# Kernel optimization log

Hardware: AMD Instinct MI355X
Metric: run time of the kernel (lower is better)

## Reference

```python
import jax, jax.numpy as jnp
from jax import lax
import numpy as np

B, S, H, DIN, BIN, NH, NL = 32, 256, 256, 16, 2, 8, 3
DH = H // NH


def setup_inputs() -> dict:
    key = jax.random.key(0)
    it = iter(jax.random.split(key, 40))
    def nrm(shape, s=0.05):
        return jax.random.normal(next(it), shape, jnp.float32) * s
    return {
        "parts": jax.random.normal(next(it), (B, S, DIN), jnp.float32),
        "bin_info": jax.random.normal(next(it), (B, BIN), jnp.float32),
        "target": jax.random.randint(next(it), (B, S), 0, S, dtype=jnp.int32),
        "pe_W1": nrm((H // 2, DIN)), "pe_b1": jnp.zeros((H // 2,), jnp.float32),
        "pe_W2": nrm((H // 2, H // 2)), "pe_b2": jnp.zeros((H // 2,), jnp.float32),
        "be_W1": nrm((H // 4, BIN)), "be_b1": jnp.zeros((H // 4,), jnp.float32),
        "be_W2": nrm((H // 4, H // 4)), "be_b2": jnp.zeros((H // 4,), jnp.float32),
        "pos_emb": nrm((S, H // 4)),
        "tr_Wqkv": nrm((NL, 3 * H, H)), "tr_bqkv": jnp.zeros((NL, 3 * H), jnp.float32),
        "tr_Wo": nrm((NL, H, H)), "tr_bo": jnp.zeros((NL, H), jnp.float32),
        "tr_ln1_g": jnp.ones((NL, H), jnp.float32), "tr_ln1_b": jnp.zeros((NL, H), jnp.float32),
        "tr_ff_W1": nrm((NL, 2 * H, H)), "tr_ff_b1": jnp.zeros((NL, 2 * H), jnp.float32),
        "tr_ff_W2": nrm((NL, H, 2 * H)), "tr_ff_b2": jnp.zeros((NL, H), jnp.float32),
        "tr_ln2_g": jnp.ones((NL, H), jnp.float32), "tr_ln2_b": jnp.zeros((NL, H), jnp.float32),
        "lstm_Wih": nrm((4 * H, H)), "lstm_Whh": nrm((4 * H, H)),
        "lstm_bih": jnp.zeros((4 * H,), jnp.float32), "lstm_bhh": jnp.zeros((4 * H,), jnp.float32),
        "ptr_W": nrm((H, H)), "ptr_b": jnp.zeros((H,), jnp.float32),
        "ptr_v": nrm((H,)),
    }


def _ln(x, g, b):
    m = x.mean(-1, keepdims=True)
    v = ((x - m) ** 2).mean(-1, keepdims=True)
    return (x - m) / jnp.sqrt(v + 1e-5) * g + b


def _forward(parts, bin_info, target, pe_W1, pe_b1, pe_W2, pe_b2,
             be_W1, be_b1, be_W2, be_b2, pos_emb,
             tr_Wqkv, tr_bqkv, tr_Wo, tr_bo, tr_ln1_g, tr_ln1_b,
             tr_ff_W1, tr_ff_b1, tr_ff_W2, tr_ff_b2, tr_ln2_g, tr_ln2_b,
             lstm_Wih, lstm_Whh, lstm_bih, lstm_bhh, ptr_W, ptr_b, ptr_v):
    # --- encode_inputs (dropout inactive in eval) ---
    p = jax.nn.relu(parts @ pe_W1.T + pe_b1) @ pe_W2.T + pe_b2            # [B,S,H/2]
    bb = jax.nn.relu(bin_info @ be_W1.T + be_b1) @ be_W2.T + be_b2        # [B,H/4]
    bb = jnp.broadcast_to(bb[:, None, :], (B, S, H // 4))
    pe = jnp.broadcast_to(pos_emb[None], (B, S, H // 4))
    x = jnp.concatenate([p, bb, pe], axis=-1)                             # [B,S,H]
    scale = 1.0 / np.sqrt(DH)
    for l in range(NL):  # post-norm TransformerEncoderLayer, relu FFN
        qkv = x @ tr_Wqkv[l].T + tr_bqkv[l]
        q, k, v = jnp.split(qkv, 3, axis=-1)
        q = q.reshape(B, S, NH, DH).transpose(0, 2, 1, 3)
        k = k.reshape(B, S, NH, DH).transpose(0, 2, 1, 3)
        v = v.reshape(B, S, NH, DH).transpose(0, 2, 1, 3)
        a = jax.nn.softmax(jnp.einsum('bhqd,bhkd->bhqk', q, k) * scale, axis=-1)
        o = jnp.einsum('bhqk,bhkd->bhqd', a, v).transpose(0, 2, 1, 3).reshape(B, S, H)
        x = _ln(x + o @ tr_Wo[l].T + tr_bo[l], tr_ln1_g[l], tr_ln1_b[l])
        ff = jax.nn.relu(x @ tr_ff_W1[l].T + tr_ff_b1[l]) @ tr_ff_W2[l].T + tr_ff_b2[l]
        x = _ln(x + ff, tr_ln2_g[l], tr_ln2_b[l])
    enc = x
    # Note: the original's inner MultiheadAttention calls never feed the
    # returned step_logits (part_logit is overwritten), so the faithful output is
    # logits[b,t,i] = v . tanh(ptr(h_t) + ptr(enc_i)), vectorized over i here.
    e_proj = enc @ ptr_W.T + ptr_b                                        # [B,S,H]
    bidx = jnp.arange(B)

    def step(carry, tgt_t):
        h, c, xin = carry
        g = xin @ lstm_Wih.T + lstm_bih + h @ lstm_Whh.T + lstm_bhh
        i, f, gg, o = jnp.split(g, 4, axis=-1)
        c = jax.nn.sigmoid(f) * c + jax.nn.sigmoid(i) * jnp.tanh(gg)
        h = jax.nn.sigmoid(o) * jnp.tanh(c)
        hp = h @ ptr_W.T + ptr_b                                          # [B,H]
        logits = jnp.tanh(hp[:, None, :] + e_proj) @ ptr_v                # [B,S]
        nxt = enc[bidx, tgt_t]                                            # teacher forcing
        return (h, c, nxt), logits

    z = jnp.zeros((B, H), jnp.float32)
    _, logits = lax.scan(step, (z, z, z), target.T)                       # [S,B,S]
    return logits.transpose(1, 0, 2)                                      # [B,S,S]


def reference(parts, bin_info, target, pe_W1, pe_b1, pe_W2, pe_b2,
              be_W1, be_b1, be_W2, be_b2, pos_emb,
              tr_Wqkv, tr_bqkv, tr_Wo, tr_bo, tr_ln1_g, tr_ln1_b,
              tr_ff_W1, tr_ff_b1, tr_ff_W2, tr_ff_b2, tr_ln2_g, tr_ln2_b,
              lstm_Wih, lstm_Whh, lstm_bih, lstm_bhh, ptr_W, ptr_b, ptr_v):
    return _forward(parts, bin_info, target, pe_W1, pe_b1, pe_W2, pe_b2,
                    be_W1, be_b1, be_W2, be_b2, pos_emb,
                    tr_Wqkv, tr_bqkv, tr_Wo, tr_bo, tr_ln1_g, tr_ln1_b,
                    tr_ff_W1, tr_ff_b1, tr_ff_W2, tr_ff_b2, tr_ln2_g, tr_ln2_b,
                    lstm_Wih, lstm_Whh, lstm_bih, lstm_bhh, ptr_W, ptr_b, ptr_v)
```

## Files before the change

kernel.cpp:

```cpp
#include <hip/hip_runtime.h>
#include <cstddef>

#define DEV __device__ __forceinline__

DEV float fexp2(float x) { return __builtin_amdgcn_exp2f(x); }
DEV float frcp(float x)  { return __builtin_amdgcn_rcpf(x); }
DEV float fsigm(float x) { return frcp(1.0f + fexp2(-1.44269504f * x)); }
DEV float ftanh_(float x){ return 1.0f - 2.0f * frcp(1.0f + fexp2(2.88539008f * x)); }

typedef _Float16 h2t __attribute__((ext_vector_type(2)));
typedef _Float16 v8h __attribute__((ext_vector_type(8)));
typedef float v4f __attribute__((ext_vector_type(4)));
union U32H2 { unsigned int u; h2t h; };
DEV h2t u2h(unsigned int u) { U32H2 x; x.u = u; return x.h; }

template <int BM, int BN, bool RELU, bool OUTF16>
__global__ __launch_bounds__(256) void hgemm_kernel(
    const _Float16* __restrict__ A, const _Float16* __restrict__ W,
    const float* __restrict__ bias1, const float* __restrict__ bias2,
    void* __restrict__ Cout, int M, int N, int K)
{
    constexpr int MT = BM / 32;
    constexpr int NT = BN / 32;
    constexpr int RA = BM / 64;
    constexpr int RB = BN / 64;
    __shared__ _Float16 As[BM * 32];
    __shared__ _Float16 Bs[BN * 32];

    const int tid = threadIdx.x;
    const int lane = tid & 63;
    const int lm = lane & 15, lq = lane >> 4;
    const int wrow = ((tid >> 6) & 1) * (BM / 2);
    const int wcol = (tid >> 7) * (BN / 2);
    const int m0 = blockIdx.x * BM, n0 = blockIdx.y * BN;
    const _Float16* Ab = A + (size_t)m0 * K;
    const _Float16* Wb = W + (size_t)n0 * K;

    v4f acc[MT][NT];
#pragma unroll
    for (int i = 0; i < MT; ++i)
#pragma unroll
        for (int j = 0; j < NT; ++j) acc[i][j] = (v4f){0.f, 0.f, 0.f, 0.f};

    const int rowS = tid >> 2, qS = tid & 3;

    uint4 ra[RA], rb[RB];
#pragma unroll
    for (int r = 0; r < RA; ++r)
        ra[r] = *(const uint4*)(Ab + (size_t)(rowS + 64 * r) * K + qS * 8);
#pragma unroll
    for (int r = 0; r < RB; ++r)
        rb[r] = *(const uint4*)(Wb + (size_t)(rowS + 64 * r) * K + qS * 8);

    for (int k0 = 0; k0 < K; k0 += 32) {
        __syncthreads();
#pragma unroll
        for (int r = 0; r < RA; ++r)
            *(uint4*)(As + (size_t)(tid + 256 * r) * 8) = ra[r];
#pragma unroll
        for (int r = 0; r < RB; ++r)
            *(uint4*)(Bs + (size_t)(tid + 256 * r) * 8) = rb[r];
        __syncthreads();
        int kn = k0 + 32;
        if (kn < K) {
#pragma unroll
            for (int r = 0; r < RA; ++r)
                ra[r] = *(const uint4*)(Ab + (size_t)(rowS + 64 * r) * K + kn + qS * 8);
#pragma unroll
            for (int r = 0; r < RB; ++r)
                rb[r] = *(const uint4*)(Wb + (size_t)(rowS + 64 * r) * K + kn + qS * 8);
        }
        v8h af[MT], bf[NT];
#pragma unroll
        for (int i = 0; i < MT; ++i)
            af[i] = *(const v8h*)(As + (size_t)(wrow + i * 16 + lm) * 32 + lq * 8);
#pragma unroll
        for (int j = 0; j < NT; ++j)
            bf[j] = *(const v8h*)(Bs + (size_t)(wcol + j * 16 + lm) * 32 + lq * 8);
#pragma unroll
        for (int i = 0; i < MT; ++i)
#pragma unroll
            for (int j = 0; j < NT; ++j)
                acc[i][j] = __builtin_amdgcn_mfma_f32_16x16x32_f16(
                    af[i], bf[j], acc[i][j], 0, 0, 0);
    }

#pragma unroll
    for (int j = 0; j < NT; ++j) {
        int col = n0 + wcol + j * 16 + lm;
        float bv = bias1[col];
        if (bias2) bv += bias2[col];
#pragma unroll
        for (int i = 0; i < MT; ++i) {
            int rbase = m0 + wrow + i * 16 + lq * 4;
#pragma unroll
            for (int rg = 0; rg < 4; ++rg) {
                float vv = acc[i][j][rg] + bv;
                if (RELU) vv = fmaxf(vv, 0.f);
                if (OUTF16)
                    ((_Float16*)Cout)[(size_t)(rbase + rg) * N + col] = (_Float16)vv;
                else
                    ((float*)Cout)[(size_t)(rbase + rg) * N + col] = vv;
            }
        }
    }
}

__global__ __launch_bounds__(256) void hgemm_ln_kernel(
    const _Float16* __restrict__ A, const _Float16* __restrict__ W,
    const float* __restrict__ bias, const float* __restrict__ gamma,
    const float* __restrict__ beta, float* __restrict__ X,
    _Float16* __restrict__ X16, int K)
{
    constexpr int BM = 64, BN = 256, MT = 2, NT = 8, RA = 1, RB = 4;
    __shared__ _Float16 As[BM * 32];
    __shared__ _Float16 Bs[BN * 32];
    __shared__ float redS[2][BM][2];

    const int tid = threadIdx.x;
    const int lane = tid & 63;
    const int lm = lane & 15, lq = lane >> 4;
    const int wrow = ((tid >> 6) & 1) * 32;
    const int wcol = (tid >> 7) * 128;
    const int half = tid >> 7;
    const int m0 = blockIdx.x * BM;
    const _Float16* Ab = A + (size_t)m0 * K;

    v4f acc[MT][NT];
#pragma unroll
    for (int i = 0; i < MT; ++i)
#pragma unroll
        for (int j = 0; j < NT; ++j) acc[i][j] = (v4f){0.f, 0.f, 0.f, 0.f};

    const int rowS = tid >> 2, qS = tid & 3;

    uint4 ra[RA], rb[RB];
#pragma unroll
    for (int r = 0; r < RA; ++r)
        ra[r] = *(const uint4*)(Ab + (size_t)(rowS + 64 * r) * K + qS * 8);
#pragma unroll
    for (int r = 0; r < RB; ++r)
        rb[r] = *(const uint4*)(W + (size_t)(rowS + 64 * r) * K + qS * 8);

    for (int k0 = 0; k0 < K; k0 += 32) {
        __syncthreads();
#pragma unroll
        for (int r = 0; r < RA; ++r)
            *(uint4*)(As + (size_t)(tid + 256 * r) * 8) = ra[r];
#pragma unroll
        for (int r = 0; r < RB; ++r)
            *(uint4*)(Bs + (size_t)(tid + 256 * r) * 8) = rb[r];
        __syncthreads();
        int kn = k0 + 32;
        if (kn < K) {
#pragma unroll
            for (int r = 0; r < RA; ++r)
                ra[r] = *(const uint4*)(Ab + (size_t)(rowS + 64 * r) * K + kn + qS * 8);
#pragma unroll
            for (int r = 0; r < RB; ++r)
                rb[r] = *(const uint4*)(W + (size_t)(rowS + 64 * r) * K + kn + qS * 8);
        }
        v8h af[MT], bf[NT];
#pragma unroll
        for (int i = 0; i < MT; ++i)
            af[i] = *(const v8h*)(As + (size_t)(wrow + i * 16 + lm) * 32 + lq * 8);
#pragma unroll
        for (int j = 0; j < NT; ++j)
            bf[j] = *(const v8h*)(Bs + (size_t)(wcol + j * 16 + lm) * 32 + lq * 8);
#pragma unroll
        for (int i = 0; i < MT; ++i)
#pragma unroll
            for (int j = 0; j < NT; ++j)
                acc[i][j] = __builtin_amdgcn_mfma_f32_16x16x32_f16(
                    af[i], bf[j], acc[i][j], 0, 0, 0);
    }

    float s[MT][4], s2[MT][4];
#pragma unroll
    for (int i = 0; i < MT; ++i)
#pragma unroll
        for (int rg = 0; rg < 4; ++rg) { s[i][rg] = 0.f; s2[i][rg] = 0.f; }
#pragma unroll
    for (int j = 0; j < NT; ++j) {
        int col = wcol + j * 16 + lm;
        float bv = bias[col];
#pragma unroll
        for (int i = 0; i < MT; ++i) {
            int rbase = m0 + wrow + i * 16 + lq * 4;
#pragma unroll
            for (int rg = 0; rg < 4; ++rg) {
                float y = acc[i][j][rg] + bv + X[(size_t)(rbase + rg) * 256 + col];
                acc[i][j][rg] = y;
                s[i][rg] += y;
                s2[i][rg] += y * y;
            }
        }
    }
#pragma unroll
    for (int i = 0; i < MT; ++i)
#pragma unroll
        for (int rg = 0; rg < 4; ++rg) {
            float a = s[i][rg], b2 = s2[i][rg];
#pragma unroll
            for (int m = 1; m < 16; m <<= 1) {
                a += __shfl_xor(a, m);
                b2 += __shfl_xor(b2, m);
            }
            if (lm == 0) {
                int rloc = wrow + i * 16 + lq * 4 + rg;
                redS[half][rloc][0] = a;
                redS[half][rloc][1] = b2;
            }
        }
    __syncthreads();
#pragma unroll
    for (int i = 0; i < MT; ++i) {
#pragma unroll
        for (int rg = 0; rg < 4; ++rg) {
            int rloc = wrow + i * 16 + lq * 4 + rg;
            float st = redS[0][rloc][0] + redS[1][rloc][0];
            float s2t = redS[0][rloc][1] + redS[1][rloc][1];
            float mean = st * (1.f / 256.f);
            float var = s2t * (1.f / 256.f) - mean * mean;
            float inv = rsqrtf(var + 1e-5f);
            size_t rowb = (size_t)(m0 + rloc) * 256;
#pragma unroll
            for (int j = 0; j < NT; ++j) {
                int col = wcol + j * 16 + lm;
                float o = (acc[i][j][rg] - mean) * inv * gamma[col] + beta[col];
                X[rowb + col] = o;
                X16[rowb + col] = (_Float16)o;
            }
        }
    }
}

__global__ __launch_bounds__(256) void cvt_fused_kernel(
    const float* __restrict__ s0, const float* __restrict__ s1,
    const float* __restrict__ s2, const float* __restrict__ s3,
    const float* __restrict__ s4, const float* __restrict__ s5,
    _Float16* __restrict__ dst,
    const float* __restrict__ Whh, unsigned int* __restrict__ WB,
    const float* __restrict__ bih, const float* __restrict__ bhh,
    float* __restrict__ PB)
{
    if (blockIdx.x < 7424) {
        int i = blockIdx.x * 256 + threadIdx.x;
        if (i >= 1900544) return;
        float val;
        if (i < 589824)       val = s0[i];
        else if (i < 786432)  val = s1[i - 589824];
        else if (i < 1179648) val = s2[i - 786432];
        else if (i < 1572864) val = s3[i - 1179648];
        else if (i < 1835008) {
            int idx = i - 1572864;
            int rp = idx >> 8, k = idx & 255;
            int j = rp >> 2, g = rp & 3;
            val = s4[(g * 256 + j) * 256 + k];
        }
        else                  val = s5[i - 1835008];
        dst[i] = (_Float16)val;
    } else {
        int idx = (blockIdx.x - 7424) * 256 + threadIdx.x;
        if (idx < 1024) {
            int j = idx >> 2, g = idx & 3;
            PB[idx] = bih[g * 256 + j] + bhh[g * 256 + j];
        }
        int l = idx & 3;
        int gt = idx >> 2;
        int tid = gt & 511;
        int q = gt >> 9;
        int i, c;
        if (q < 8)       { i = q >> 1; c = q & 1; }
        else if (q < 52) { int qq = q - 8; i = qq / 11; c = 2 + qq % 11; }
        else             { int qq = q - 52; c = 13 + (qq >> 2); i = qq & 3; }
        int r = ((tid & 255) << 2) + i;
        int k = ((tid >> 8) << 7) + (c << 3) + (l << 1);
        _Float16 lo = (_Float16)Whh[r * 256 + k];
        _Float16 hi = (_Float16)Whh[r * 256 + k + 1];
        U32H2 x; x.h = h2t{lo, hi};
        WB[idx] = x.u;
    }
}

__global__ __launch_bounds__(128) void part_enc_kernel(
    const float* __restrict__ parts, const float* __restrict__ W1,
    const float* __restrict__ b1, const float* __restrict__ W2,
    const float* __restrict__ b2, const float* __restrict__ bin_info,
    const float* __restrict__ be_W1, const float* __restrict__ be_b1,
    const float* __restrict__ be_W2, const float* __restrict__ be_b2,
    const float* __restrict__ pos_emb, float* __restrict__ X,
    _Float16* __restrict__ X16)
{
    __shared__ float W2s[128][129];
    __shared__ float h1[128];
    __shared__ float pin[16];
    __shared__ float h1b[64];
    __shared__ float bb_s[64];
    int tid = threadIdx.x;
    int b = blockIdx.x >> 3, s0 = (blockIdx.x & 7) * 32;
    for (int l = 0; l < 128; ++l) W2s[l][tid] = W2[l * 128 + tid];
    {
        float x0 = bin_info[b * 2], x1 = bin_info[b * 2 + 1];
        if (tid < 64)
            h1b[tid] = fmaxf(be_W1[tid * 2] * x0 + be_W1[tid * 2 + 1] * x1
                             + be_b1[tid], 0.f);
        __syncthreads();
        if (tid < 64) {
            float a = be_b2[tid];
#pragma unroll 4
            for (int e = 0; e < 64; ++e) a += be_W2[tid * 64 + e] * h1b[e];
            bb_s[tid] = a;
        }
        __syncthreads();
    }
    float w1r[16];
#pragma unroll
    for (int k = 0; k < 16; ++k) w1r[k] = W1[tid * 16 + k];
    float bias1v = b1[tid], bias2v = b2[tid];
    for (int si = 0; si < 32; ++si) {
        int s = s0 + si;
        size_t row = (size_t)b * 256 + s;
        if (tid < 16) pin[tid] = parts[row * 16 + tid];
        __syncthreads();
        float h = bias1v;
#pragma unroll
        for (int k = 0; k < 16; ++k) h += w1r[k] * pin[k];
        h1[tid] = fmaxf(h, 0.f);
        __syncthreads();
        float acc = bias2v;
#pragma unroll 4
        for (int e = 0; e < 128; ++e) acc += W2s[tid][e] * h1[e];
        X[row * 256 + tid] = acc;
        X16[row * 256 + tid] = (_Float16)acc;
        if (tid < 64) {
            float bbv = bb_s[tid];
            float pev = pos_emb[s * 64 + tid];
            X[row * 256 + 128 + tid] = bbv;
            X[row * 256 + 192 + tid] = pev;
            X16[row * 256 + 128 + tid] = (_Float16)bbv;
            X16[row * 256 + 192 + tid] = (_Float16)pev;
        }
        __syncthreads();
    }
}

__global__ __launch_bounds__(256) void attn_mfma_kernel(
    const _Float16* __restrict__ QKV, _Float16* __restrict__ O16)
{
    int bh = blockIdx.x;
    int b = bh >> 3, h = bh & 7;
    const int tid = threadIdx.x;
    const int w = tid >> 6;
    const int lane = tid & 63;
    const int lm = lane & 15, lq = lane >> 4;
    const float c_se = 0.17677669529663687f * 1.44269504f;

    __shared__ _Float16 Ks[4][256][8];
    __shared__ _Float16 Vt[32][264];
    __shared__ _Float16 Ps[4][16][264];

    const _Float16* qkvb = QKV + (size_t)(b * 256) * 768 + h * 32;
    {
        int s = tid;
        const _Float16* kr = qkvb + (size_t)s * 768 + 256;
#pragma unroll
        for (int c = 0; c < 4; ++c)
            *(uint4*)&Ks[c][s][0] = *(const uint4*)(kr + c * 8);
        const _Float16* vr = qkvb + (size_t)s * 768 + 512;
        _Float16 vtmp[32];
        *(uint4*)&vtmp[0]  = *(const uint4*)(vr);
        *(uint4*)&vtmp[8]  = *(const uint4*)(vr + 8);
        *(uint4*)&vtmp[16] = *(const uint4*)(vr + 16);
        *(uint4*)&vtmp[24] = *(const uint4*)(vr + 24);
#pragma unroll
        for (int d = 0; d < 32; ++d) Vt[d][s] = vtmp[d];
    }
    __syncthreads();

#pragma unroll 1
    for (int st = 0; st < 4; ++st) {
        int rt = w * 4 + st;
        v8h qf = *(const v8h*)(QKV + (size_t)(b * 256 + rt * 16 + lm) * 768
                               + h * 32 + lq * 8);
        v4f acc[16];
#pragma unroll
        for (int ct = 0; ct < 16; ++ct) {
            v8h kf = *(const v8h*)&Ks[lq][ct * 16 + lm][0];
            acc[ct] = __builtin_amdgcn_mfma_f32_16x16x32_f16(
                qf, kf, (v4f){0.f, 0.f, 0.f, 0.f}, 0, 0, 0);
        }
        float sminv[4];
#pragma unroll
        for (int r = 0; r < 4; ++r) {
            float m = acc[0][r];
#pragma unroll
            for (int ct = 1; ct < 16; ++ct) m = fmaxf(m, acc[ct][r]);
#pragma unroll
            for (int msk = 1; msk < 16; msk <<= 1)
                m = fmaxf(m, __shfl_xor(m, msk));
            float ssum = 0.f;
#pragma unroll
            for (int ct = 0; ct < 16; ++ct) {
                float e = fexp2((acc[ct][r] - m) * c_se);
                acc[ct][r] = e;
                ssum += e;
            }
#pragma unroll
            for (int msk = 1; msk < 16; msk <<= 1)
                ssum += __shfl_xor(ssum, msk);
            sminv[r] = frcp(ssum);
        }
#pragma unroll
        for (int ct = 0; ct < 16; ++ct)
#pragma unroll
            for (int r = 0; r < 4; ++r)
                Ps[w][lq * 4 + r][ct * 16 + lm] =
                    (_Float16)(acc[ct][r] * sminv[r]);
#pragma unroll
        for (int dt = 0; dt < 2; ++dt) {
            v4f o = (v4f){0.f, 0.f, 0.f, 0.f};
#pragma unroll
            for (int jc = 0; jc < 8; ++jc) {
                v8h pf = *(const v8h*)&Ps[w][lm][jc * 32 + lq * 8];
                v8h vf = *(const v8h*)&Vt[dt * 16 + lm][jc * 32 + lq * 8];
                o = __builtin_amdgcn_mfma_f32_16x16x32_f16(pf, vf, o, 0, 0, 0);
            }
#pragma unroll
            for (int r = 0; r < 4; ++r)
                O16[(size_t)(b * 256 + rt * 16 + lq * 4 + r) * 256
                    + h * 32 + dt * 16 + lm] = (_Float16)o[r];
        }
    }
}

__global__ __launch_bounds__(256) void gather_kernel(
    const float* __restrict__ X, const int* __restrict__ target,
    _Float16* __restrict__ Xg16)
{
    int row = blockIdx.x;
    int b = row >> 8, t = row & 255;
    int d = threadIdx.x;
    float val = 0.f;
    if (t > 0) {
        int src = target[b * 256 + t - 1];
        val = X[((size_t)b * 256 + src) * 256 + d];
    }
    Xg16[(size_t)row * 256 + d] = (_Float16)val;
}

__global__ __launch_bounds__(512) void lstm_kernel(
    const _Float16* __restrict__ g_in, const uint4* __restrict__ WB4,
    _Float16* __restrict__ HALL16)
{
    const int b = blockIdx.x;
    const int tid = threadIdx.x;
    const int kh = tid >> 8, j4 = tid & 255;

    __shared__ uint4 WL4[4096];
    __shared__ float gpart[2][1024];
    __shared__ uint4 h2v[32];
    unsigned int* h2_s = (unsigned int*)h2v;

#pragma unroll
    for (int g = 0; g < 8; ++g) WL4[g * 512 + tid] = WB4[g * 512 + tid];
    uint4 wr[44];
#pragma unroll
    for (int q = 0; q < 44; ++q) wr[q] = WB4[(8 + q) * 512 + tid];
    if (tid < 128) h2_s[tid] = 0u;

    const _Float16* ginb = g_in + (size_t)b * 256 * 1024;
    uint2 gi = make_uint2(0u, 0u);
    if (tid < 256) gi = *(const uint2*)(ginb + tid * 4);
    float c_state = 0.f;
    const uint4* SW4 = WB4 + 52 * 512;
    __syncthreads();

    for (int t = 0; t < 256; ++t) {
        uint4 sw[12];
#pragma unroll
        for (int q = 0; q < 4; ++q) sw[q] = SW4[q * 512 + tid];

        unsigned int hword = h2_s[(kh << 6) + (tid & 63)];

        float acc[4] = {0.f, 0.f, 0.f, 0.f};
#pragma unroll
        for (int c = 0; c < 16; ++c) {
            if (c == 2) {
#pragma unroll
                for (int q = 4; q < 8; ++q) sw[q] = SW4[q * 512 + tid];
            }
            if (c == 6) {
#pragma unroll
                for (int q = 8; q < 12; ++q) sw[q] = SW4[q * 512 + tid];
            }
            h2t hx = u2h((unsigned int)__builtin_amdgcn_readlane((int)hword, 4 * c + 0));
            h2t hy = u2h((unsigned int)__builtin_amdgcn_readlane((int)hword, 4 * c + 1));
            h2t hz = u2h((unsigned int)__builtin_amdgcn_readlane((int)hword, 4 * c + 2));
            h2t hw = u2h((unsigned int)__builtin_amdgcn_readlane((int)hword, 4 * c + 3));
#pragma unroll
            for (int i = 0; i < 4; ++i) {
                uint4 w = (c < 2)  ? WL4[((i << 1) + c) * 512 + tid]
                        : (c < 13) ? wr[i * 11 + (c - 2)]
                                   : sw[((c - 13) << 2) + i];
                acc[i] = __builtin_amdgcn_fdot2(u2h(w.x), hx, acc[i], false);
                acc[i] = __builtin_amdgcn_fdot2(u2h(w.y), hy, acc[i], false);
                acc[i] = __builtin_amdgcn_fdot2(u2h(w.z), hz, acc[i], false);
                acc[i] = __builtin_amdgcn_fdot2(u2h(w.w), hw, acc[i], false);
            }
        }
        *(float4*)&gpart[kh][j4 << 2] = make_float4(acc[0], acc[1], acc[2], acc[3]);
        __syncthreads();

        if (tid < 256) {
            int j = tid;
            h2t p0 = u2h(gi.x), p1 = u2h(gi.y);
            float ig = (float)p0.x + gpart[0][j]       + gpart[1][j];
            float fg = (float)p0.y + gpart[0][j + 256] + gpart[1][j + 256];
            float gg = (float)p1.x + gpart[0][j + 512] + gpart[1][j + 512];
            float og = (float)p1.y + gpart[0][j + 768] + gpart[1][j + 768];
            c_state = fsigm(fg) * c_state + fsigm(ig) * ftanh_(gg);
            float h = fsigm(og) * ftanh_(c_state);
            HALL16[((size_t)(b * 256 + t)) * 256 + j] = (_Float16)h;
            U32H2 hxp; hxp.h = h2t{(_Float16)h, (_Float16)0.f};
            unsigned int hu = hxp.u & 0xffffu;
            unsigned int other = (unsigned int)__shfl_xor((int)hu, 1);
            if ((j & 1) == 0) h2_s[j >> 1] = hu | (other << 16);
            int tn = (t < 255) ? (t + 1) : 255;
            gi = *(const uint2*)(ginb + (size_t)tn * 1024 + j * 4);
        }
        __syncthreads();
    }
}

__global__ __launch_bounds__(256) void pointer_kernel(
    const float* __restrict__ HP, const float* __restrict__ EP,
    const float* __restrict__ v, float* __restrict__ out)
{
    int b = blockIdx.z, tt = blockIdx.y, it = blockIdx.x;
    __shared__ float hp_s[16][260];
    __shared__ float ep_s[16][260];
    __shared__ float v_s[256];
    __shared__ float red[4];
    int tid = threadIdx.x;
    const float cs = 2.88539008f;
    const float* hpb = HP + ((size_t)b * 256 + tt * 16) * 256;
    const float* epb = EP + ((size_t)b * 256 + it * 16) * 256;
#pragma unroll
    for (int l = 0; l < 4; ++l) {
        int idx = tid + l * 256;
        int r = idx >> 6, c4 = idx & 63;
        float4 hv = *(const float4*)(hpb + r * 256 + c4 * 4);
        hv.x *= cs; hv.y *= cs; hv.z *= cs; hv.w *= cs;
        *(float4*)&hp_s[r][c4 * 4] = hv;
        float4 ev = *(const float4*)(epb + r * 256 + c4 * 4);
        ev.x *= cs; ev.y *= cs; ev.z *= cs; ev.w *= cs;
        *(float4*)&ep_s[r][c4 * 4] = ev;
    }
    float vv = v[tid];
    v_s[tid] = vv;
    float vp = vv;
#pragma unroll
    for (int m = 1; m < 64; m <<= 1) vp += __shfl_xor(vp, m);
    if ((tid & 63) == 0) red[tid >> 6] = vp;
    __syncthreads();
    float vsum = red[0] + red[1] + red[2] + red[3];
    int tl = tid >> 4, il = tid & 15;
    float acc = 0.f;
#pragma unroll 4
    for (int d = 0; d < 256; ++d) {
        float sval = hp_s[tl][d] + ep_s[il][d];
        float r = frcp(1.0f + fexp2(sval));
        acc = fmaf(v_s[d], r, acc);
    }
    out[((size_t)b * 256 + tt * 16 + tl) * 256 + it * 16 + il] =
        vsum - 2.0f * acc;
}

extern "C" void kernel_launch(void* const* d_in, const int* in_sizes, int n_in,
                              void* d_out, int out_size, void* d_ws, size_t ws_size,
                              hipStream_t stream)
{
    const float* parts    = (const float*)d_in[0];
    const float* bin_info = (const float*)d_in[1];
    const int*   target   = (const int*)d_in[2];
    const float* pe_W1 = (const float*)d_in[3];
    const float* pe_b1 = (const float*)d_in[4];
    const float* pe_W2 = (const float*)d_in[5];
    const float* pe_b2 = (const float*)d_in[6];
    const float* be_W1 = (const float*)d_in[7];
    const float* be_b1 = (const float*)d_in[8];
    const float* be_W2 = (const float*)d_in[9];
    const float* be_b2 = (const float*)d_in[10];
    const float* pos_emb = (const float*)d_in[11];
    const float* tr_Wqkv = (const float*)d_in[12];
    const float* tr_bqkv = (const float*)d_in[13];
    const float* tr_Wo   = (const float*)d_in[14];
    const float* tr_bo   = (const float*)d_in[15];
    const float* tr_ln1_g = (const float*)d_in[16];
    const float* tr_ln1_b = (const float*)d_in[17];
    const float* tr_ff_W1 = (const float*)d_in[18];
    const float* tr_ff_b1 = (const float*)d_in[19];
    const float* tr_ff_W2 = (const float*)d_in[20];
    const float* tr_ff_b2 = (const float*)d_in[21];
    const float* tr_ln2_g = (const float*)d_in[22];
    const float* tr_ln2_b = (const float*)d_in[23];
    const float* lstm_Wih = (const float*)d_in[24];
    const float* lstm_Whh = (const float*)d_in[25];
    const float* lstm_bih = (const float*)d_in[26];
    const float* lstm_bhh = (const float*)d_in[27];
    const float* ptr_W = (const float*)d_in[28];
    const float* ptr_b = (const float*)d_in[29];
    const float* ptr_v = (const float*)d_in[30];

    float* ws = (float*)d_ws;
    float* X     = ws;
    float* S1    = X + 2097152;
    float* CF32  = S1 + 8388608;
    float* EPROJ = CF32 + 2097152;
    float* X16f  = EPROJ + 2097152;
    float* S2f   = X16f + 1048576;
    float* W16f  = S2f + 1048576;
    float* WBf   = W16f + 1048576;
    float* BBuf  = WBf + 131072;
    float* PB    = BBuf + 2048;

    _Float16* X16    = (_Float16*)X16f;
    _Float16* Xg16   = X16;
    _Float16* S2h    = (_Float16*)S2f;
    _Float16* HALL16 = S2h;
    _Float16* S1h    = (_Float16*)S1;
    _Float16* W16    = (_Float16*)W16f;
    _Float16* Wqkv16 = W16;
    _Float16* Wo16   = Wqkv16 + 589824;
    _Float16* Wff116 = Wo16 + 196608;
    _Float16* Wff216 = Wff116 + 393216;
    _Float16* Wih16  = Wff216 + 393216;
    _Float16* WpW16  = Wih16 + 262144;

    cvt_fused_kernel<<<7936, 256, 0, stream>>>(
        tr_Wqkv, tr_Wo, tr_ff_W1, tr_ff_W2, lstm_Wih, ptr_W, W16,
        lstm_Whh, (unsigned int*)WBf, lstm_bih, lstm_bhh, PB);

    part_enc_kernel<<<256, 128, 0, stream>>>(parts, pe_W1, pe_b1, pe_W2, pe_b2,
                                             bin_info, be_W1, be_b1, be_W2, be_b2,
                                             pos_emb, X, X16);

    for (int l = 0; l < 3; ++l) {
        hgemm_kernel<64, 128, false, true><<<dim3(128, 6), 256, 0, stream>>>(
            X16, Wqkv16 + (size_t)l * 196608, tr_bqkv + l * 768, nullptr,
            S1h, 8192, 768, 256);
        attn_mfma_kernel<<<256, 256, 0, stream>>>(S1h, S2h);
        hgemm_ln_kernel<<<128, 256, 0, stream>>>(
            S2h, Wo16 + (size_t)l * 65536, tr_bo + l * 256,
            tr_ln1_g + l * 256, tr_ln1_b + l * 256, X, X16, 256);
        hgemm_kernel<64, 128, true, true><<<dim3(128, 4), 256, 0, stream>>>(
            X16, Wff116 + (size_t)l * 131072, tr_ff_b1 + l * 512, nullptr,
            S1h, 8192, 512, 256);
        hgemm_ln_kernel<<<128, 256, 0, stream>>>(
            S1h, Wff216 + (size_t)l * 131072, tr_ff_b2 + l * 256,
            tr_ln2_g + l * 256, tr_ln2_b + l * 256, X, X16, 512);
    }

    hgemm_kernel<64, 64, false, false><<<dim3(128, 4), 256, 0, stream>>>(
        X16, WpW16, ptr_b, nullptr, EPROJ, 8192, 256, 256);
    gather_kernel<<<8192, 256, 0, stream>>>(X, target, Xg16);
    hgemm_kernel<64, 128, false, true><<<dim3(128, 8), 256, 0, stream>>>(
        Xg16, Wih16, PB, nullptr, S1h, 8192, 1024, 256);
    lstm_kernel<<<32, 512, 0, stream>>>(S1h, (const uint4*)WBf, HALL16);
    hgemm_kernel<64, 64, false, false><<<dim3(128, 4), 256, 0, stream>>>(
        HALL16, WpW16, ptr_b, nullptr, CF32, 8192, 256, 256);
    pointer_kernel<<<dim3(16, 16, 32), 256, 0, stream>>>(CF32, EPROJ, ptr_v,
                                                         (float*)d_out);
}
```

Before: 1.177 ms.

## Compute LSTM recurrent matvec with MFMA using register-resident weight fragments

Replaces the per-step fdot2 matvec in the LSTM recurrence, whose weights were split across LDS, registers and repeated global loads, with MFMA 16x16x32 f16 instructions. The full Whh is repacked into MFMA B-fragment layout and held in registers (64 uint4 per thread). Each step broadcasts h as the A operand and keeps only row 0 of the MFMA output. This removes the per-step global weight streaming and the two-way partial-sum reduction. In exchange it wastes 15/16 of the MFMA rows and raises register pressure considerably.

```diff
diff --git a/kernel.cpp b/kernel.cpp
--- a/kernel.cpp
+++ b/kernel.cpp
@@ -266,18 +266,16 @@
             int j = idx >> 2, g = idx & 3;
             PB[idx] = bih[g * 256 + j] + bhh[g * 256 + j];
         }
-        int l = idx & 3;
-        int gt = idx >> 2;
-        int tid = gt & 511;
-        int q = gt >> 9;
-        int i, c;
-        if (q < 8)       { i = q >> 1; c = q & 1; }
-        else if (q < 52) { int qq = q - 8; i = qq / 11; c = 2 + qq % 11; }
-        else             { int qq = q - 52; c = 13 + (qq >> 2); i = qq & 3; }
-        int r = ((tid & 255) << 2) + i;
-        int k = ((tid >> 8) << 7) + (c << 3) + (l << 1);
-        _Float16 lo = (_Float16)Whh[r * 256 + k];
-        _Float16 hi = (_Float16)Whh[r * 256 + k + 1];
+        int wd   = idx & 3;
+        int lane = (idx >> 2) & 63;
+        int kt   = (idx >> 8) & 7;
+        int jt   = (idx >> 11) & 7;
+        int w    = (idx >> 14) & 7;
+        int n = w * 128 + jt * 16 + (lane & 15);
+        int src_r = (n & 3) * 256 + (n >> 2);
+        int k = kt * 32 + ((lane >> 4) << 3) + (wd << 1);
+        _Float16 lo = (_Float16)Whh[src_r * 256 + k];
+        _Float16 hi = (_Float16)Whh[src_r * 256 + k + 1];
         U32H2 x; x.h = h2t{lo, hi};
         WB[idx] = x.u;
     }
@@ -455,70 +453,60 @@
 {
     const int b = blockIdx.x;
     const int tid = threadIdx.x;
-    const int kh = tid >> 8, j4 = tid & 255;
-
-    __shared__ uint4 WL4[4096];
-    __shared__ float gpart[2][1024];
+    const int w = tid >> 6;
+    const int lane = tid & 63;
+    const int lq = lane >> 4;
+
+    __shared__ float gf[1024];
     __shared__ uint4 h2v[32];
     unsigned int* h2_s = (unsigned int*)h2v;
 
-#pragma unroll
-    for (int g = 0; g < 8; ++g) WL4[g * 512 + tid] = WB4[g * 512 + tid];
-    uint4 wr[44];
-#pragma unroll
-    for (int q = 0; q < 44; ++q) wr[q] = WB4[(8 + q) * 512 + tid];
+    uint4 wf[8][8];
+#pragma unroll
+    for (int jt = 0; jt < 8; ++jt)
+#pragma unroll
+        for (int kt = 0; kt < 8; ++kt)
+            wf[jt][kt] = WB4[((((w << 3) + jt) << 3) + kt) * 64 + lane];
+
     if (tid < 128) h2_s[tid] = 0u;
 
     const _Float16* ginb = g_in + (size_t)b * 256 * 1024;
     uint2 gi = make_uint2(0u, 0u);
     if (tid < 256) gi = *(const uint2*)(ginb + tid * 4);
     float c_state = 0.f;
-    const uint4* SW4 = WB4 + 52 * 512;
     __syncthreads();
 
     for (int t = 0; t < 256; ++t) {
-        uint4 sw[12];
-#pragma unroll
-        for (int q = 0; q < 4; ++q) sw[q] = SW4[q * 512 + tid];
-
-        unsigned int hword = h2_s[(kh << 6) + (tid & 63)];
-
-        float acc[4] = {0.f, 0.f, 0.f, 0.f};
-#pragma unroll
-        for (int c = 0; c < 16; ++c) {
-            if (c == 2) {
-#pragma unroll
-                for (int q = 4; q < 8; ++q) sw[q] = SW4[q * 512 + tid];
-            }
-            if (c == 6) {
-#pragma unroll
-                for (int q = 8; q < 12; ++q) sw[q] = SW4[q * 512 + tid];
-            }
-            h2t hx = u2h((unsigned int)__builtin_amdgcn_readlane((int)hword, 4 * c + 0));
-            h2t hy = u2h((unsigned int)__builtin_amdgcn_readlane((int)hword, 4 * c + 1));
-            h2t hz = u2h((unsigned int)__builtin_amdgcn_readlane((int)hword, 4 * c + 2));
-            h2t hw = u2h((unsigned int)__builtin_amdgcn_readlane((int)hword, 4 * c + 3));
-#pragma unroll
-            for (int i = 0; i < 4; ++i) {
-                uint4 w = (c < 2)  ? WL4[((i << 1) + c) * 512 + tid]
-                        : (c < 13) ? wr[i * 11 + (c - 2)]
-                                   : sw[((c - 13) << 2) + i];
-                acc[i] = __builtin_amdgcn_fdot2(u2h(w.x), hx, acc[i], false);
-                acc[i] = __builtin_amdgcn_fdot2(u2h(w.y), hy, acc[i], false);
-                acc[i] = __builtin_amdgcn_fdot2(u2h(w.z), hz, acc[i], false);
-                acc[i] = __builtin_amdgcn_fdot2(u2h(w.w), hw, acc[i], false);
-            }
-        }
-        *(float4*)&gpart[kh][j4 << 2] = make_float4(acc[0], acc[1], acc[2], acc[3]);
+        uint4 ha[8];
+#pragma unroll
+        for (int kt = 0; kt < 8; ++kt) ha[kt] = h2v[kt * 4 + lq];
+
+        v4f acc[8];
+#pragma unroll
+        for (int jt = 0; jt < 8; ++jt) acc[jt] = (v4f){0.f, 0.f, 0.f, 0.f};
+#pragma unroll
+        for (int kt = 0; kt < 8; ++kt) {
+            v8h av = *(v8h*)&ha[kt];
+#pragma unroll
+            for (int jt = 0; jt < 8; ++jt)
+                acc[jt] = __builtin_amdgcn_mfma_f32_16x16x32_f16(
+                    av, *(v8h*)&wf[jt][kt], acc[jt], 0, 0, 0);
+        }
+        if (lane < 16) {
+#pragma unroll
+            for (int jt = 0; jt < 8; ++jt)
+                gf[(w << 7) + (jt << 4) + lane] = acc[jt][0];
+        }
         __syncthreads();
 
         if (tid < 256) {
             int j = tid;
+            float4 gv = *(const float4*)&gf[j << 2];
             h2t p0 = u2h(gi.x), p1 = u2h(gi.y);
-            float ig = (float)p0.x + gpart[0][j]       + gpart[1][j];
-            float fg = (float)p0.y + gpart[0][j + 256] + gpart[1][j + 256];
-            float gg = (float)p1.x + gpart[0][j + 512] + gpart[1][j + 512];
-            float og = (float)p1.y + gpart[0][j + 768] + gpart[1][j + 768];
+            float ig = (float)p0.x + gv.x;
+            float fg = (float)p0.y + gv.y;
+            float gg = (float)p1.x + gv.z;
+            float og = (float)p1.y + gv.w;
             c_state = fsigm(fg) * c_state + fsigm(ig) * ftanh_(gg);
             float h = fsigm(og) * ftanh_(c_state);
             HALL16[((size_t)(b * 256 + t)) * 256 + j] = (_Float16)h;
```

Result: slower. 1.729 ms (+46.9%).
